# Performance work log

Measured on AMD Instinct MI355X. Metric: run time of the kernel, lower is better.

Reference implementation:

```python
import jax, jax.numpy as jnp
import numpy as np

MAX_ANTS = 16  # padded max draws per (batch, neuron); ragged draws masked with -1
BS, N_IN, N_OUT = 32, 4096, 4096


def setup_inputs() -> dict:
    key = jax.random.key(0)
    k1, k2 = jax.random.split(key)
    # integer ant counts per (batch, input neuron), in [0, MAX_ANTS)
    x = jax.random.randint(k1, (BS, N_IN), 0, MAX_ANTS, dtype=jnp.int32)
    # positive weights (original init is uniform 1/n_outputs; random positive is general)
    weights = jax.random.uniform(k2, (N_IN, N_OUT), dtype=jnp.float32, minval=0.01, maxval=1.0)
    return {"x": x, "weights": weights}


def reference(x, weights):
    """Vectorized equivalent of ACOLayer.forward.

    Original: for each batch b and input neuron i with count c = x[b, i] > 0,
    draw c iid categorical samples from row-normalized weights[i].
    Here: inverse-CDF sampling, padded to MAX_ANTS draws, invalid slots = -1.
    Returns int32 [bs, n_in, MAX_ANTS].
    """
    probs = weights / weights.sum(axis=1, keepdims=True)   # normalize()
    cdf = jnp.cumsum(probs, axis=1)                        # [n_in, n_out]
    bs, n_in = x.shape
    n_out = weights.shape[1]
    u = jax.random.uniform(jax.random.key(42), (bs, n_in, MAX_ANTS), dtype=weights.dtype)
    # group draws by input neuron so each row's CDF is searched once
    u_rows = u.transpose(1, 0, 2).reshape(n_in, bs * MAX_ANTS)  # [n_in, bs*MAX]
    idx = jax.vmap(jnp.searchsorted)(cdf, u_rows)               # inverse-CDF draw
    idx = jnp.minimum(idx, n_out - 1).astype(jnp.int32)
    idx = idx.reshape(n_in, bs, MAX_ANTS).transpose(1, 0, 2)    # [bs, n_in, MAX]
    valid = jnp.arange(MAX_ANTS, dtype=x.dtype)[None, None, :] < x[:, :, None]
    return jnp.where(valid, idx, -1)
```

## Files before the change

kernel.cpp:

```cpp
#include <hip/hip_runtime.h>
#include <stdint.h>


#define N_IN    4096
#define N_OUT   4096
#define BS      32
#define MAX_A   16
#define THREADS 256
#define HALF    1048576u
#define WIN     64

__device__ __forceinline__ int padi(int j) { return j + (j >> 5); }

__device__ __forceinline__ uint32_t rotl32(uint32_t x, uint32_t r) {
    return (x << r) | (x >> (32u - r));
}

__device__ __forceinline__ void threefry2x32_42(uint32_t x0, uint32_t x1,
                                                uint32_t& o0, uint32_t& o1) {
    const uint32_t k0 = 0u, k1 = 42u;
    const uint32_t k2 = k0 ^ k1 ^ 0x1BD11BDAu;
    x0 += k0; x1 += k1;
#define TF_R(r) { x0 += x1; x1 = rotl32(x1, (r)); x1 ^= x0; }
    TF_R(13) TF_R(15) TF_R(26) TF_R(6)
    x0 += k1; x1 += k2 + 1u;
    TF_R(17) TF_R(29) TF_R(16) TF_R(24)
    x0 += k2; x1 += k0 + 2u;
    TF_R(13) TF_R(15) TF_R(26) TF_R(6)
    x0 += k0; x1 += k1 + 3u;
    TF_R(17) TF_R(29) TF_R(16) TF_R(24)
    x0 += k1; x1 += k2 + 4u;
    TF_R(13) TF_R(15) TF_R(26) TF_R(6)
    x0 += k2; x1 += k0 + 5u;
#undef TF_R
    o0 = x0; o1 = x1;
}

__device__ __forceinline__ float bits_to_uniform(uint32_t b) {
    uint32_t f = (b >> 9) | 0x3f800000u;
    float r;
    __builtin_memcpy(&r, &f, 4);
    return r - 1.0f;
}

__global__ __launch_bounds__(THREADS, 8)
void aco_sample_kernel(const int* __restrict__ x,
                       const float* __restrict__ w,
                       int* __restrict__ out) {
    __shared__ float cdf[N_OUT + (N_OUT >> 5)];
    __shared__ float wsum[4];
    __shared__ int   xc[BS];

    const int row  = blockIdx.x;
    const int t    = threadIdx.x;
    const int lane = t & 63;
    const int wid  = t >> 6;

    const float4* wrow = (const float4*)(w + (size_t)row * N_OUT);
    float4 v0 = wrow[t * 4 + 0];
    float4 v1 = wrow[t * 4 + 1];
    float4 v2 = wrow[t * 4 + 2];
    float4 v3 = wrow[t * 4 + 3];

    if (t < BS) xc[t] = x[t * N_IN + row];

    const int bb = t >> 4;
    const int aa = t & 15;
    const uint32_t j0 = (uint32_t)(bb * (N_IN * MAX_A) + row * MAX_A + aa);
    const uint32_t j1 = j0 + HALF;
    uint32_t o0, o1, p0, p1;
    threefry2x32_42(0u, j0, o0, o1);
    threefry2x32_42(0u, j1, p0, p1);
    const float u0 = bits_to_uniform(o0 ^ o1);
    const float u1 = bits_to_uniform(p0 ^ p1);

    float s = 0.f;
    s += v0.x; s += v0.y; s += v0.z; s += v0.w;
    s += v1.x; s += v1.y; s += v1.z; s += v1.w;
    s += v2.x; s += v2.y; s += v2.z; s += v2.w;
    s += v3.x; s += v3.y; s += v3.z; s += v3.w;
    const float my_total = s;

    float incl = my_total;
    #pragma unroll
    for (int d = 1; d < 64; d <<= 1) {
        float n = __shfl_up(incl, d, 64);
        if (lane >= d) incl += n;
    }
    if (lane == 63) wsum[wid] = incl;
    __syncthreads();

    const float4 ws = *(const float4*)wsum;
    const float total = ws.x + ws.y + ws.z + ws.w;
    float wprefix = 0.f;
    if (wid > 0) wprefix += ws.x;
    if (wid > 1) wprefix += ws.y;
    if (wid > 2) wprefix += ws.z;
    const float chunk_prefix = wprefix + incl - my_total;

    {
        const int base = t * 16;
        float r = chunk_prefix;
        r += v0.x; cdf[padi(base +  0)] = r;
        r += v0.y; cdf[padi(base +  1)] = r;
        r += v0.z; cdf[padi(base +  2)] = r;
        r += v0.w; cdf[padi(base +  3)] = r;
        r += v1.x; cdf[padi(base +  4)] = r;
        r += v1.y; cdf[padi(base +  5)] = r;
        r += v1.z; cdf[padi(base +  6)] = r;
        r += v1.w; cdf[padi(base +  7)] = r;
        r += v2.x; cdf[padi(base +  8)] = r;
        r += v2.y; cdf[padi(base +  9)] = r;
        r += v2.z; cdf[padi(base + 10)] = r;
        r += v2.w; cdf[padi(base + 11)] = r;
        r += v3.x; cdf[padi(base + 12)] = r;
        r += v3.y; cdf[padi(base + 13)] = r;
        r += v3.z; cdf[padi(base + 14)] = r;
        r += v3.w; cdf[padi(base + 15)] = r;
    }
    __syncthreads();

    const float t0 = u0 * total;
    const float t1 = u1 * total;

    const int i0 = (int)(u0 * (float)N_OUT);
    const int i1 = (int)(u1 * (float)N_OUT);
    int lo0 = i0 - WIN; if (lo0 < 0) lo0 = 0;
    int hi0 = i0 + WIN; if (hi0 > N_OUT) hi0 = N_OUT;
    int lo1 = i1 - WIN; if (lo1 < 0) lo1 = 0;
    int hi1 = i1 + WIN; if (hi1 > N_OUT) hi1 = N_OUT;

    const bool ok0 = (lo0 == 0     || cdf[padi(lo0 - 1)] <  t0) &&
                     (hi0 == N_OUT || cdf[padi(hi0 - 1)] >= t0);
    const bool ok1 = (lo1 == 0     || cdf[padi(lo1 - 1)] <  t1) &&
                     (hi1 == N_OUT || cdf[padi(hi1 - 1)] >= t1);

    if (ok0 && ok1) {
        #pragma unroll
        for (int it = 0; it < 7; ++it) {
            const int m0 = (lo0 + hi0) >> 1;
            const int m1 = (lo1 + hi1) >> 1;
            const float f0 = cdf[padi(m0)];
            const float f1 = cdf[padi(m1)];
            if (f0 < t0) lo0 = m0 + 1; else hi0 = m0;
            if (f1 < t1) lo1 = m1 + 1; else hi1 = m1;
        }
    } else {
        lo0 = 0; hi0 = N_OUT; lo1 = 0; hi1 = N_OUT;
        #pragma unroll
        for (int it = 0; it < 12; ++it) {
            const int m0 = (lo0 + hi0) >> 1;
            const int m1 = (lo1 + hi1) >> 1;
            const float f0 = cdf[padi(m0)];
            const float f1 = cdf[padi(m1)];
            if (f0 < t0) lo0 = m0 + 1; else hi0 = m0;
            if (f1 < t1) lo1 = m1 + 1; else hi1 = m1;
        }
    }
    const int idx0 = lo0 < N_OUT ? lo0 : N_OUT - 1;
    const int idx1 = lo1 < N_OUT ? lo1 : N_OUT - 1;

    out[j0] = (aa < xc[bb])      ? idx0 : -1;
    out[j1] = (aa < xc[bb + 16]) ? idx1 : -1;
}

extern "C" void kernel_launch(void* const* d_in, const int* in_sizes, int n_in,
                              void* d_out, int out_size, void* d_ws, size_t ws_size,
                              hipStream_t stream) {
    const int*   x;
    const float* w;
    if (in_sizes[0] == BS * N_IN) { x = (const int*)d_in[0]; w = (const float*)d_in[1]; }
    else                          { x = (const int*)d_in[1]; w = (const float*)d_in[0]; }
    aco_sample_kernel<<<N_IN, THREADS, 0, stream>>>(x, w, (int*)d_out);
}
```

Before: 19.88 us.

## Process two weight rows per block with both rows' loads issued up front

Each block now handles two input-neuron rows, and the grid is halved. Both rows' weights are loaded into registers at the start, so the second row's global load is in flight while the first row is scanned and searched. The shared CDF buffer is reused, with a barrier between the two rows. The cost is higher register pressure (32 extra floats per thread), which may lower occupancy under the 8-blocks launch bound, and fewer blocks to spread across the GPU.

```diff
diff --git a/kernel.cpp b/kernel.cpp
--- a/kernel.cpp
+++ b/kernel.cpp
@@ -9,6 +9,7 @@
 #define THREADS 256
 #define HALF    1048576u
 #define WIN     64
+#define GRID    (N_IN / 2)
 
 __device__ __forceinline__ int padi(int j) { return j + (j >> 5); }
 
@@ -43,36 +44,11 @@
     return r - 1.0f;
 }
 
-__global__ __launch_bounds__(THREADS, 8)
-void aco_sample_kernel(const int* __restrict__ x,
-                       const float* __restrict__ w,
-                       int* __restrict__ out) {
-    __shared__ float cdf[N_OUT + (N_OUT >> 5)];
-    __shared__ float wsum[4];
-    __shared__ int   xc[BS];
-
-    const int row  = blockIdx.x;
-    const int t    = threadIdx.x;
-    const int lane = t & 63;
-    const int wid  = t >> 6;
-
-    const float4* wrow = (const float4*)(w + (size_t)row * N_OUT);
-    float4 v0 = wrow[t * 4 + 0];
-    float4 v1 = wrow[t * 4 + 1];
-    float4 v2 = wrow[t * 4 + 2];
-    float4 v3 = wrow[t * 4 + 3];
-
-    if (t < BS) xc[t] = x[t * N_IN + row];
-
-    const int bb = t >> 4;
-    const int aa = t & 15;
-    const uint32_t j0 = (uint32_t)(bb * (N_IN * MAX_A) + row * MAX_A + aa);
-    const uint32_t j1 = j0 + HALF;
-    uint32_t o0, o1, p0, p1;
-    threefry2x32_42(0u, j0, o0, o1);
-    threefry2x32_42(0u, j1, p0, p1);
-    const float u0 = bits_to_uniform(o0 ^ o1);
-    const float u1 = bits_to_uniform(p0 ^ p1);
+__device__ __forceinline__ void process_row(
+        float* cdf, float* wsum, const int* xcr,
+        float4 v0, float4 v1, float4 v2, float4 v3,
+        int row, int t, int lane, int wid, int bb, int aa,
+        uint32_t j0, float u0, float u1, int* __restrict__ out) {
 
     float s = 0.f;
     s += v0.x; s += v0.y; s += v0.z; s += v0.w;
@@ -160,8 +136,60 @@
     const int idx0 = lo0 < N_OUT ? lo0 : N_OUT - 1;
     const int idx1 = lo1 < N_OUT ? lo1 : N_OUT - 1;
 
-    out[j0] = (aa < xc[bb])      ? idx0 : -1;
-    out[j1] = (aa < xc[bb + 16]) ? idx1 : -1;
+    out[j0]        = (aa < xcr[bb])      ? idx0 : -1;
+    out[j0 + HALF] = (aa < xcr[bb + 16]) ? idx1 : -1;
+}
+
+__global__ __launch_bounds__(THREADS, 8)
+void aco_sample_kernel(const int* __restrict__ x,
+                       const float* __restrict__ w,
+                       int* __restrict__ out) {
+    __shared__ float cdf[N_OUT + (N_OUT >> 5)];
+    __shared__ float wsum[4];
+    __shared__ int   xc[2][BS];
+
+    const int t    = threadIdx.x;
+    const int lane = t & 63;
+    const int wid  = t >> 6;
+    const int bb   = t >> 4;
+    const int aa   = t & 15;
+    const int row0 = blockIdx.x;
+    const int row1 = blockIdx.x + GRID;
+
+    const float4* wr0 = (const float4*)(w + (size_t)row0 * N_OUT);
+    float4 a0 = wr0[t * 4 + 0];
+    float4 a1 = wr0[t * 4 + 1];
+    float4 a2 = wr0[t * 4 + 2];
+    float4 a3 = wr0[t * 4 + 3];
+    const float4* wr1 = (const float4*)(w + (size_t)row1 * N_OUT);
+    float4 b0 = wr1[t * 4 + 0];
+    float4 b1 = wr1[t * 4 + 1];
+    float4 b2 = wr1[t * 4 + 2];
+    float4 b3 = wr1[t * 4 + 3];
+
+    if (t < BS)          xc[0][t]      = x[t * N_IN + row0];
+    else if (t < 2 * BS) xc[1][t - BS] = x[(t - BS) * N_IN + row1];
+
+    const uint32_t jA = (uint32_t)(bb * (N_IN * MAX_A) + row0 * MAX_A + aa);
+    uint32_t o0, o1, p0, p1;
+    threefry2x32_42(0u, jA, o0, o1);
+    threefry2x32_42(0u, jA + HALF, p0, p1);
+    const float uA0 = bits_to_uniform(o0 ^ o1);
+    const float uA1 = bits_to_uniform(p0 ^ p1);
+
+    process_row(cdf, wsum, xc[0], a0, a1, a2, a3,
+                row0, t, lane, wid, bb, aa, jA, uA0, uA1, out);
+
+    const uint32_t jB = (uint32_t)(bb * (N_IN * MAX_A) + row1 * MAX_A + aa);
+    threefry2x32_42(0u, jB, o0, o1);
+    threefry2x32_42(0u, jB + HALF, p0, p1);
+    const float uB0 = bits_to_uniform(o0 ^ o1);
+    const float uB1 = bits_to_uniform(p0 ^ p1);
+
+    __syncthreads();
+
+    process_row(cdf, wsum, xc[1], b0, b1, b2, b3,
+                row1, t, lane, wid, bb, aa, jB, uB0, uB1, out);
 }
 
 extern "C" void kernel_launch(void* const* d_in, const int* in_sizes, int n_in,
@@ -171,5 +199,5 @@
     const float* w;
     if (in_sizes[0] == BS * N_IN) { x = (const int*)d_in[0]; w = (const float*)d_in[1]; }
     else                          { x = (const int*)d_in[1]; w = (const float*)d_in[0]; }
-    aco_sample_kernel<<<N_IN, THREADS, 0, stream>>>(x, w, (int*)d_out);
-}
+    aco_sample_kernel<<<GRID, THREADS, 0, stream>>>(x, w, (int*)d_out);
+}
```

Measured after the change: 22.98 us. 1.16x slower.
